# Performance work log

Hardware: AMD Instinct MI355X
Metric: run time of the kernel (lower is better)

The kernel has to match this reference:

```python
import jax, jax.numpy as jnp
import numpy as np

N_NODES = 100000
N_EDGES = 640000
IN_FEATS = 128
OUT_FEATS = 128


def setup_inputs() -> dict:
    key = jax.random.key(0)
    k1, k2, k3, k4 = jax.random.split(key, 4)
    feature = jax.random.normal(k1, (N_NODES, IN_FEATS), dtype=jnp.float32)
    edge_index = jax.random.randint(k2, (2, N_EDGES), 0, N_NODES, dtype=jnp.int64)
    # Linear params (W stored as [in, out] so out = h @ W + b, same math as torch Linear)
    W = jax.random.normal(k3, (IN_FEATS, OUT_FEATS), dtype=jnp.float32) / np.sqrt(IN_FEATS)
    b = jax.random.normal(k4, (OUT_FEATS,), dtype=jnp.float32) * 0.01
    return {"feature": feature, "edge_index": edge_index, "W": W, "b": b}


def reference(feature, edge_index, W, b):
    src, dst = edge_index[0], edge_index[1]
    # copy_src: gather source-node features along edges -> [E, in]
    msgs = feature[src]
    # sum reduce at destination nodes -> [N, in]
    h = jax.ops.segment_sum(msgs, dst, num_segments=N_NODES)
    # post-aggregation linear
    return h @ W + b
```

## Files before the change

### kernel.cpp

```cpp
#include <hip/hip_runtime.h>

#define N_NODES 100000
#define N_EDGES 640000
#define FEATS   128
#define CAP     64

typedef __attribute__((ext_vector_type(8))) short short8;
typedef __attribute__((ext_vector_type(4))) float f32x4;

static __device__ __forceinline__ unsigned short f2bf(float f) {
  union { float f; unsigned u; } c; c.f = f;
  unsigned u = c.u + 0x7fffu + ((c.u >> 16) & 1u);
  return (unsigned short)(u >> 16);
}
static __device__ __forceinline__ float asf(unsigned u) {
  union { unsigned u; float f; } c; c.u = u;
  return c.f;
}

__global__ __launch_bounds__(256) void fused_prep(
    const float* __restrict__ feature, const float* __restrict__ W,
    const int* __restrict__ edge,
    unsigned short* __restrict__ feat_bf, unsigned short* __restrict__ WT,
    int* __restrict__ cnt, int* __restrict__ bucket) {
  int b = blockIdx.x;
  if (b < 6250) {
    size_t g = (size_t)b * 256 + threadIdx.x;
    const float4* s = (const float4*)feature + g * 2;
    float4 a = s[0], c = s[1];
    unsigned short o[8] = {f2bf(a.x), f2bf(a.y), f2bf(a.z), f2bf(a.w),
                           f2bf(c.x), f2bf(c.y), f2bf(c.z), f2bf(c.w)};
    *(short8*)(feat_bf + g * 8) = *(const short8*)o;
  } else if (b < 6314) {
    int g = (b - 6250) * 256 + threadIdx.x;
    int k = g >> 7, n = g & 127;
    WT[n * 128 + k] = f2bf(W[g]);
  } else {
    int e = (b - 6314) * 256 + threadIdx.x;
    if (e < N_EDGES) {
      int d = edge[N_EDGES + e];
      int s = edge[e];
      int slot = atomicAdd(&cnt[d], 1);
      if (slot < CAP) bucket[d * CAP + slot] = s;
    }
  }
}

__global__ __launch_bounds__(256) void aggregate_kernel(
    const unsigned short* __restrict__ feat,
    const int* __restrict__ cnt, const int* __restrict__ bucket,
    unsigned short* __restrict__ h) {
  int g    = blockIdx.x * 256 + threadIdx.x;
  int node = g >> 4;
  int lane = g & 15;
  int deg  = min(cnt[node], CAP);
  const int* eb = bucket + node * CAP;

  float a0 = 0.f, a1 = 0.f, a2 = 0.f, a3 = 0.f;
  float a4 = 0.f, a5 = 0.f, a6 = 0.f, a7 = 0.f;

  int i = 0;
  for (; i + 3 < deg; i += 4) {
    int s0 = eb[i], s1 = eb[i + 1], s2 = eb[i + 2], s3 = eb[i + 3];
    uint4 p0 = *(const uint4*)(feat + (size_t)s0 * FEATS + lane * 8);
    uint4 p1 = *(const uint4*)(feat + (size_t)s1 * FEATS + lane * 8);
    uint4 p2 = *(const uint4*)(feat + (size_t)s2 * FEATS + lane * 8);
    uint4 p3 = *(const uint4*)(feat + (size_t)s3 * FEATS + lane * 8);
    a0 += asf(p0.x << 16) + asf(p1.x << 16) + asf(p2.x << 16) + asf(p3.x << 16);
    a1 += asf(p0.x & 0xffff0000u) + asf(p1.x & 0xffff0000u) + asf(p2.x & 0xffff0000u) + asf(p3.x & 0xffff0000u);
    a2 += asf(p0.y << 16) + asf(p1.y << 16) + asf(p2.y << 16) + asf(p3.y << 16);
    a3 += asf(p0.y & 0xffff0000u) + asf(p1.y & 0xffff0000u) + asf(p2.y & 0xffff0000u) + asf(p3.y & 0xffff0000u);
    a4 += asf(p0.z << 16) + asf(p1.z << 16) + asf(p2.z << 16) + asf(p3.z << 16);
    a5 += asf(p0.z & 0xffff0000u) + asf(p1.z & 0xffff0000u) + asf(p2.z & 0xffff0000u) + asf(p3.z & 0xffff0000u);
    a6 += asf(p0.w << 16) + asf(p1.w << 16) + asf(p2.w << 16) + asf(p3.w << 16);
    a7 += asf(p0.w & 0xffff0000u) + asf(p1.w & 0xffff0000u) + asf(p2.w & 0xffff0000u) + asf(p3.w & 0xffff0000u);
  }
  for (; i < deg; ++i) {
    int s = eb[i];
    uint4 p = *(const uint4*)(feat + (size_t)s * FEATS + lane * 8);
    a0 += asf(p.x << 16);
    a1 += asf(p.x & 0xffff0000u);
    a2 += asf(p.y << 16);
    a3 += asf(p.y & 0xffff0000u);
    a4 += asf(p.z << 16);
    a5 += asf(p.z & 0xffff0000u);
    a6 += asf(p.w << 16);
    a7 += asf(p.w & 0xffff0000u);
  }

  uint4 o;
  o.x = (unsigned)f2bf(a0) | ((unsigned)f2bf(a1) << 16);
  o.y = (unsigned)f2bf(a2) | ((unsigned)f2bf(a3) << 16);
  o.z = (unsigned)f2bf(a4) | ((unsigned)f2bf(a5) << 16);
  o.w = (unsigned)f2bf(a6) | ((unsigned)f2bf(a7) << 16);
  *(uint4*)(h + (size_t)node * FEATS + lane * 8) = o;
}


#define LDSK 136

__global__ __launch_bounds__(256) void gemm_mfma(
    const unsigned short* __restrict__ hbf,
    const unsigned short* __restrict__ WT,
    const float* __restrict__ bias,
    float* __restrict__ out) {
  __shared__ unsigned short WTs[128 * LDSK];

  #pragma unroll
  for (int i = 0; i < 8; ++i) {
    int c = threadIdx.x + i * 256;
    int n = c >> 4, j = c & 15;
    *(short8*)&WTs[n * LDSK + j * 8] = *(const short8*)(WT + n * 128 + j * 8);
  }
  __syncthreads();

  const int w    = threadIdx.x >> 6;
  const int lane = threadIdx.x & 63;
  const int ln15 = lane & 15;
  const int quad = lane >> 4;
  const int row_base = blockIdx.x * 128 + w * 32;

  f32x4 acc[2][8] = {};

  #pragma unroll
  for (int kb = 0; kb < 4; ++kb) {
    int kofs = kb * 32 + quad * 8;
    short8 a0 = *(const short8*)(hbf + (size_t)(row_base + ln15) * FEATS + kofs);
    short8 a1 = *(const short8*)(hbf + (size_t)(row_base + 16 + ln15) * FEATS + kofs);
    #pragma unroll
    for (int ct = 0; ct < 8; ++ct) {
      short8 b = *(const short8*)&WTs[(ct * 16 + ln15) * LDSK + kofs];
      acc[0][ct] = __builtin_amdgcn_mfma_f32_16x16x32_bf16(a0, b, acc[0][ct], 0, 0, 0);
      acc[1][ct] = __builtin_amdgcn_mfma_f32_16x16x32_bf16(a1, b, acc[1][ct], 0, 0, 0);
    }
  }

  #pragma unroll
  for (int t = 0; t < 2; ++t) {
    #pragma unroll
    for (int ct = 0; ct < 8; ++ct) {
      int col = ct * 16 + ln15;
      float bv = bias[col];
      #pragma unroll
      for (int r = 0; r < 4; ++r) {
        int row = row_base + t * 16 + quad * 4 + r;
        if (row < N_NODES)
          out[(size_t)row * FEATS + col] = acc[t][ct][r] + bv;
      }
    }
  }
}


extern "C" void kernel_launch(void* const* d_in, const int* in_sizes, int n_in,
                              void* d_out, int out_size, void* d_ws, size_t ws_size,
                              hipStream_t stream) {
  const float* feature = (const float*)d_in[0];
  const int*   edge    = (const int*)d_in[1];
  const float* W       = (const float*)d_in[2];
  const float* bias    = (const float*)d_in[3];
  float*       out     = (float*)d_out;

  char* ws = (char*)d_ws;
  int* cnt    = (int*)(ws);
  int* bucket = (int*)(ws + (1 << 20));
  unsigned short* WT      = (unsigned short*)(ws + (27 << 20));
  unsigned short* feat_bf = (unsigned short*)(ws + (28 << 20));
  unsigned short* h_bf    = (unsigned short*)(ws + (54 << 20));

  hipMemsetAsync(cnt, 0, N_NODES * sizeof(int), stream);

  fused_prep<<<6314 + (N_EDGES + 255) / 256, 256, 0, stream>>>(
      feature, W, edge, feat_bf, WT, cnt, bucket);

  aggregate_kernel<<<N_NODES * 16 / 256, 256, 0, stream>>>(
      feat_bf, cnt, bucket, h_bf);

  gemm_mfma<<<(N_NODES + 127) / 128, 256, 0, stream>>>(h_bf, WT, bias, out);
}
```

Baseline: 191.6 us.

## Apply linear transform before aggregation and fuse GEMM with edge bucketing

```diff
diff --git a/kernel.cpp b/kernel.cpp
--- a/kernel.cpp
+++ b/kernel.cpp
@@ -4,6 +4,9 @@
 #define N_EDGES 640000
 #define FEATS   128
 #define CAP     64
+#define SCAT_BLOCKS 625
+#define GEMM_BLOCKS 782
+#define LDSK 136
 
 typedef __attribute__((ext_vector_type(8))) short short8;
 typedef __attribute__((ext_vector_type(4))) float f32x4;
@@ -18,99 +21,40 @@
   return c.f;
 }
 
-__global__ __launch_bounds__(256) void fused_prep(
+static __device__ __forceinline__ short8 load_a8(const float* __restrict__ p) {
+  float4 x = ((const float4*)p)[0];
+  float4 y = ((const float4*)p)[1];
+  unsigned short o[8] = {f2bf(x.x), f2bf(x.y), f2bf(x.z), f2bf(x.w),
+                         f2bf(y.x), f2bf(y.y), f2bf(y.z), f2bf(y.w)};
+  return *(const short8*)o;
+}
+
+__global__ __launch_bounds__(256) void gemm_scatter(
     const float* __restrict__ feature, const float* __restrict__ W,
     const int* __restrict__ edge,
-    unsigned short* __restrict__ feat_bf, unsigned short* __restrict__ WT,
-    int* __restrict__ cnt, int* __restrict__ bucket) {
-  int b = blockIdx.x;
-  if (b < 6250) {
-    size_t g = (size_t)b * 256 + threadIdx.x;
-    const float4* s = (const float4*)feature + g * 2;
-    float4 a = s[0], c = s[1];
-    unsigned short o[8] = {f2bf(a.x), f2bf(a.y), f2bf(a.z), f2bf(a.w),
-                           f2bf(c.x), f2bf(c.y), f2bf(c.z), f2bf(c.w)};
-    *(short8*)(feat_bf + g * 8) = *(const short8*)o;
-  } else if (b < 6314) {
-    int g = (b - 6250) * 256 + threadIdx.x;
-    int k = g >> 7, n = g & 127;
-    WT[n * 128 + k] = f2bf(W[g]);
-  } else {
-    int e = (b - 6314) * 256 + threadIdx.x;
-    if (e < N_EDGES) {
-      int d = edge[N_EDGES + e];
-      int s = edge[e];
-      int slot = atomicAdd(&cnt[d], 1);
-      if (slot < CAP) bucket[d * CAP + slot] = s;
-    }
-  }
-}
-
-__global__ __launch_bounds__(256) void aggregate_kernel(
-    const unsigned short* __restrict__ feat,
-    const int* __restrict__ cnt, const int* __restrict__ bucket,
-    unsigned short* __restrict__ h) {
-  int g    = blockIdx.x * 256 + threadIdx.x;
-  int node = g >> 4;
-  int lane = g & 15;
-  int deg  = min(cnt[node], CAP);
-  const int* eb = bucket + node * CAP;
-
-  float a0 = 0.f, a1 = 0.f, a2 = 0.f, a3 = 0.f;
-  float a4 = 0.f, a5 = 0.f, a6 = 0.f, a7 = 0.f;
-
-  int i = 0;
-  for (; i + 3 < deg; i += 4) {
-    int s0 = eb[i], s1 = eb[i + 1], s2 = eb[i + 2], s3 = eb[i + 3];
-    uint4 p0 = *(const uint4*)(feat + (size_t)s0 * FEATS + lane * 8);
-    uint4 p1 = *(const uint4*)(feat + (size_t)s1 * FEATS + lane * 8);
-    uint4 p2 = *(const uint4*)(feat + (size_t)s2 * FEATS + lane * 8);
-    uint4 p3 = *(const uint4*)(feat + (size_t)s3 * FEATS + lane * 8);
-    a0 += asf(p0.x << 16) + asf(p1.x << 16) + asf(p2.x << 16) + asf(p3.x << 16);
-    a1 += asf(p0.x & 0xffff0000u) + asf(p1.x & 0xffff0000u) + asf(p2.x & 0xffff0000u) + asf(p3.x & 0xffff0000u);
-    a2 += asf(p0.y << 16) + asf(p1.y << 16) + asf(p2.y << 16) + asf(p3.y << 16);
-    a3 += asf(p0.y & 0xffff0000u) + asf(p1.y & 0xffff0000u) + asf(p2.y & 0xffff0000u) + asf(p3.y & 0xffff0000u);
-    a4 += asf(p0.z << 16) + asf(p1.z << 16) + asf(p2.z << 16) + asf(p3.z << 16);
-    a5 += asf(p0.z & 0xffff0000u) + asf(p1.z & 0xffff0000u) + asf(p2.z & 0xffff0000u) + asf(p3.z & 0xffff0000u);
-    a6 += asf(p0.w << 16) + asf(p1.w << 16) + asf(p2.w << 16) + asf(p3.w << 16);
-    a7 += asf(p0.w & 0xffff0000u) + asf(p1.w & 0xffff0000u) + asf(p2.w & 0xffff0000u) + asf(p3.w & 0xffff0000u);
-  }
-  for (; i < deg; ++i) {
-    int s = eb[i];
-    uint4 p = *(const uint4*)(feat + (size_t)s * FEATS + lane * 8);
-    a0 += asf(p.x << 16);
-    a1 += asf(p.x & 0xffff0000u);
-    a2 += asf(p.y << 16);
-    a3 += asf(p.y & 0xffff0000u);
-    a4 += asf(p.z << 16);
-    a5 += asf(p.z & 0xffff0000u);
-    a6 += asf(p.w << 16);
-    a7 += asf(p.w & 0xffff0000u);
+    int* __restrict__ cnt, int* __restrict__ bucket,
+    unsigned short* __restrict__ Y) {
+  if (blockIdx.x < SCAT_BLOCKS) {
+    int t = blockIdx.x * 256 + threadIdx.x;
+    int4 s4 = *(const int4*)(edge + 4 * t);
+    int4 d4 = *(const int4*)(edge + N_EDGES + 4 * t);
+    int sl0 = atomicAdd(&cnt[d4.x], 1);
+    int sl1 = atomicAdd(&cnt[d4.y], 1);
+    int sl2 = atomicAdd(&cnt[d4.z], 1);
+    int sl3 = atomicAdd(&cnt[d4.w], 1);
+    if (sl0 < CAP) bucket[d4.x * CAP + sl0] = s4.x;
+    if (sl1 < CAP) bucket[d4.y * CAP + sl1] = s4.y;
+    if (sl2 < CAP) bucket[d4.z * CAP + sl2] = s4.z;
+    if (sl3 < CAP) bucket[d4.w * CAP + sl3] = s4.w;
+    return;
   }
 
-  uint4 o;
-  o.x = (unsigned)f2bf(a0) | ((unsigned)f2bf(a1) << 16);
-  o.y = (unsigned)f2bf(a2) | ((unsigned)f2bf(a3) << 16);
-  o.z = (unsigned)f2bf(a4) | ((unsigned)f2bf(a5) << 16);
-  o.w = (unsigned)f2bf(a6) | ((unsigned)f2bf(a7) << 16);
-  *(uint4*)(h + (size_t)node * FEATS + lane * 8) = o;
-}
-
-
-#define LDSK 136
-
-__global__ __launch_bounds__(256) void gemm_mfma(
-    const unsigned short* __restrict__ hbf,
-    const unsigned short* __restrict__ WT,
-    const float* __restrict__ bias,
-    float* __restrict__ out) {
   __shared__ unsigned short WTs[128 * LDSK];
-
   #pragma unroll
-  for (int i = 0; i < 8; ++i) {
-    int c = threadIdx.x + i * 256;
-    int n = c >> 4, j = c & 15;
-    *(short8*)&WTs[n * LDSK + j * 8] = *(const short8*)(WT + n * 128 + j * 8);
+  for (int i = 0; i < 64; ++i) {
+    int idx = threadIdx.x + i * 256;
+    int k = idx >> 7, n = idx & 127;
+    WTs[n * LDSK + k] = f2bf(W[idx]);
   }
   __syncthreads();
 
@@ -118,15 +62,16 @@
   const int lane = threadIdx.x & 63;
   const int ln15 = lane & 15;
   const int quad = lane >> 4;
-  const int row_base = blockIdx.x * 128 + w * 32;
+  const int row_base = (blockIdx.x - SCAT_BLOCKS) * 128 + w * 32;
+  const int r0 = min(row_base + ln15, N_NODES - 1);
+  const int r1 = min(row_base + 16 + ln15, N_NODES - 1);
 
   f32x4 acc[2][8] = {};
-
   #pragma unroll
   for (int kb = 0; kb < 4; ++kb) {
     int kofs = kb * 32 + quad * 8;
-    short8 a0 = *(const short8*)(hbf + (size_t)(row_base + ln15) * FEATS + kofs);
-    short8 a1 = *(const short8*)(hbf + (size_t)(row_base + 16 + ln15) * FEATS + kofs);
+    short8 a0 = load_a8(feature + (size_t)r0 * FEATS + kofs);
+    short8 a1 = load_a8(feature + (size_t)r1 * FEATS + kofs);
     #pragma unroll
     for (int ct = 0; ct < 8; ++ct) {
       short8 b = *(const short8*)&WTs[(ct * 16 + ln15) * LDSK + kofs];
@@ -140,15 +85,62 @@
     #pragma unroll
     for (int ct = 0; ct < 8; ++ct) {
       int col = ct * 16 + ln15;
-      float bv = bias[col];
       #pragma unroll
       for (int r = 0; r < 4; ++r) {
         int row = row_base + t * 16 + quad * 4 + r;
-        if (row < N_NODES)
-          out[(size_t)row * FEATS + col] = acc[t][ct][r] + bv;
+        Y[(size_t)row * FEATS + col] = f2bf(acc[t][ct][r]);
       }
     }
   }
+}
+
+__global__ __launch_bounds__(256) void aggregate_kernel(
+    const unsigned short* __restrict__ Y,
+    const int* __restrict__ cnt, const int* __restrict__ bucket,
+    const float* __restrict__ bias, float* __restrict__ out) {
+  int g    = blockIdx.x * 256 + threadIdx.x;
+  int node = g >> 4;
+  int lane = g & 15;
+  int deg  = min(cnt[node], CAP);
+  const int* eb = bucket + node * CAP;
+
+  float a0 = 0.f, a1 = 0.f, a2 = 0.f, a3 = 0.f;
+  float a4 = 0.f, a5 = 0.f, a6 = 0.f, a7 = 0.f;
+
+  int i = 0;
+  for (; i + 3 < deg; i += 4) {
+    int s0 = eb[i], s1 = eb[i + 1], s2 = eb[i + 2], s3 = eb[i + 3];
+    uint4 p0 = *(const uint4*)(Y + (size_t)s0 * FEATS + lane * 8);
+    uint4 p1 = *(const uint4*)(Y + (size_t)s1 * FEATS + lane * 8);
+    uint4 p2 = *(const uint4*)(Y + (size_t)s2 * FEATS + lane * 8);
+    uint4 p3 = *(const uint4*)(Y + (size_t)s3 * FEATS + lane * 8);
+    a0 += asf(p0.x << 16) + asf(p1.x << 16) + asf(p2.x << 16) + asf(p3.x << 16);
+    a1 += asf(p0.x & 0xffff0000u) + asf(p1.x & 0xffff0000u) + asf(p2.x & 0xffff0000u) + asf(p3.x & 0xffff0000u);
+    a2 += asf(p0.y << 16) + asf(p1.y << 16) + asf(p2.y << 16) + asf(p3.y << 16);
+    a3 += asf(p0.y & 0xffff0000u) + asf(p1.y & 0xffff0000u) + asf(p2.y & 0xffff0000u) + asf(p3.y & 0xffff0000u);
+    a4 += asf(p0.z << 16) + asf(p1.z << 16) + asf(p2.z << 16) + asf(p3.z << 16);
+    a5 += asf(p0.z & 0xffff0000u) + asf(p1.z & 0xffff0000u) + asf(p2.z & 0xffff0000u) + asf(p3.z & 0xffff0000u);
+    a6 += asf(p0.w << 16) + asf(p1.w << 16) + asf(p2.w << 16) + asf(p3.w << 16);
+    a7 += asf(p0.w & 0xffff0000u) + asf(p1.w & 0xffff0000u) + asf(p2.w & 0xffff0000u) + asf(p3.w & 0xffff0000u);
+  }
+  for (; i < deg; ++i) {
+    int s = eb[i];
+    uint4 p = *(const uint4*)(Y + (size_t)s * FEATS + lane * 8);
+    a0 += asf(p.x << 16);
+    a1 += asf(p.x & 0xffff0000u);
+    a2 += asf(p.y << 16);
+    a3 += asf(p.y & 0xffff0000u);
+    a4 += asf(p.z << 16);
+    a5 += asf(p.z & 0xffff0000u);
+    a6 += asf(p.w << 16);
+    a7 += asf(p.w & 0xffff0000u);
+  }
+
+  const float4 b0 = ((const float4*)bias)[lane * 2];
+  const float4 b1 = ((const float4*)bias)[lane * 2 + 1];
+  float* op = out + (size_t)node * FEATS + lane * 8;
+  ((float4*)op)[0] = make_float4(a0 + b0.x, a1 + b0.y, a2 + b0.z, a3 + b0.w);
+  ((float4*)op)[1] = make_float4(a4 + b1.x, a5 + b1.y, a6 + b1.z, a7 + b1.w);
 }
 
 
@@ -164,17 +156,13 @@
   char* ws = (char*)d_ws;
   int* cnt    = (int*)(ws);
   int* bucket = (int*)(ws + (1 << 20));
-  unsigned short* WT      = (unsigned short*)(ws + (27 << 20));
-  unsigned short* feat_bf = (unsigned short*)(ws + (28 << 20));
-  unsigned short* h_bf    = (unsigned short*)(ws + (54 << 20));
+  unsigned short* Y = (unsigned short*)(ws + (27 << 20));
 
   hipMemsetAsync(cnt, 0, N_NODES * sizeof(int), stream);
 
-  fused_prep<<<6314 + (N_EDGES + 255) / 256, 256, 0, stream>>>(
-      feature, W, edge, feat_bf, WT, cnt, bucket);
+  gemm_scatter<<<SCAT_BLOCKS + GEMM_BLOCKS, 256, 0, stream>>>(
+      feature, W, edge, cnt, bucket, Y);
 
   aggregate_kernel<<<N_NODES * 16 / 256, 256, 0, stream>>>(
-      feat_bf, cnt, bucket, h_bf);
-
-  gemm_mfma<<<(N_NODES + 127) / 128, 256, 0, stream>>>(h_bf, WT, bias, out);
+      Y, cnt, bucket, bias, out);
 }
```

New measurement: 194.3 us. Within noise of the previous version (+1.4%).
